# Kernel optimization log

Hardware: AMD Instinct MI355X
Metric: run time of the kernel (lower is better)

Reference implementation:

```python
import jax, jax.numpy as jnp
import numpy as np
import math

E = 16          # num_experts
K = 2           # top_k
CAP_FACTOR = 1.25
TEMP = 1.0      # router_temperature


def setup_inputs() -> dict:
    key = jax.random.key(0)
    ks = jax.random.split(key, 4)
    B, F, H, O = 16384, 1024, 4096, 1024
    features = jax.random.normal(ks[0], (B, F), dtype=jnp.float32)
    Wg = jax.random.normal(ks[1], (E, F), dtype=jnp.float32) / np.sqrt(F)
    bg = jnp.zeros((E,), jnp.float32)
    W1 = jax.random.normal(ks[2], (E, F, H), dtype=jnp.float32) / np.sqrt(F)
    b1 = jnp.zeros((E, H), jnp.float32)
    W2 = jax.random.normal(ks[3], (E, H, O), dtype=jnp.float32) / np.sqrt(H)
    b2 = jnp.zeros((E, O), jnp.float32)
    expert_bias = jnp.zeros((E,), jnp.float32)
    return {"features": features, "Wg": Wg, "bg": bg, "W1": W1, "b1": b1,
            "W2": W2, "b2": b2, "expert_bias": expert_bias}


def reference(features, Wg, bg, W1, b1, W2, b2, expert_bias):
    B, F = features.shape
    O = W2.shape[-1]
    cap = max(1, int(math.ceil(CAP_FACTOR * B * K / E)))  # per-expert capacity

    # --- router: scores = W_g * features + expert_bias (no noise) ---
    scores = features @ Wg.T + bg + expert_bias[None, :]            # [B,E]
    topk_scores, topk_idx = jax.lax.top_k(scores, K)                # [B,K]
    topk_w = jax.nn.softmax(topk_scores / TEMP, axis=1)             # [B,K]

    # per-(token,expert) assignment and mixing weight
    onehot = topk_idx[:, :, None] == jnp.arange(E)[None, None, :]   # [B,K,E]
    assign = jnp.any(onehot, axis=1)                                # [B,E]
    w = jnp.sum(topk_w[:, :, None] * onehot.astype(topk_w.dtype), axis=1)  # [B,E]

    # capacity: first `cap` tokens (ascending index, matching torch.nonzero order)
    pos = jnp.cumsum(assign.astype(jnp.int32), axis=0) - 1          # [B,E]
    keep = assign & (pos < cap)
    pos_safe = jnp.where(keep, pos, cap)                            # dropped -> overflow slot

    # inverse map: inv[e,c] = token index filling slot c of expert e (B if empty)
    e_grid = jnp.broadcast_to(jnp.arange(E)[None, :], (B, E))
    b_grid = jnp.broadcast_to(jnp.arange(B, dtype=jnp.int32)[:, None], (B, E))
    inv = jnp.full((E, cap + 1), B, dtype=jnp.int32)
    inv = inv.at[e_grid, pos_safe].set(b_grid)[:, :cap]             # [E,cap]

    # dispatch (gather) into per-expert buffers
    feats_pad = jnp.concatenate([features, jnp.zeros((1, F), features.dtype)], axis=0)
    buf = feats_pad[inv]                                            # [E,cap,F]

    # experts: Linear -> ReLU -> Linear, batched over experts
    h = jax.nn.relu(jnp.einsum('ecf,efh->ech', buf, W1) + b1[:, None, :])
    y = jnp.einsum('ech,eho->eco', h, W2) + b2[:, None, :]          # [E,cap,O]

    # weighted combine (scatter-add back to tokens; empty slots have weight 0)
    w_pad = jnp.concatenate([w, jnp.zeros((1, E), w.dtype)], axis=0)  # [B+1,E]
    w_slot = w_pad[inv, jnp.arange(E)[:, None]]                     # [E,cap]
    out = jnp.zeros((B + 1, O), features.dtype)
    out = out.at[inv.reshape(-1)].add((w_slot[..., None] * y).reshape(-1, O))
    return out[:B]
```

## Files before the change

### kernel.cpp

```cpp
#include <hip/hip_runtime.h>
#include <math.h>


typedef __attribute__((ext_vector_type(8))) short bf16x8;
typedef __attribute__((ext_vector_type(4))) float floatx4;

static __device__ __forceinline__ unsigned short f2bf(float f) {
  union { float f; unsigned u; } v; v.f = f;
  unsigned u = v.u;
  return (unsigned short)((u + 0x7fffu + ((u >> 16) & 1u)) >> 16);
}

static __device__ __forceinline__ void gload_lds16(const void* g, void* l) {
  __builtin_amdgcn_global_load_lds(
      (const __attribute__((address_space(1))) unsigned int*)g,
      (__attribute__((address_space(3))) unsigned int*)l, 16, 0, 0);
}

__global__ void k_cvt_bf16(const float* __restrict__ src,
                           unsigned short* __restrict__ dst, long n4) {
  long i = (long)blockIdx.x * blockDim.x + threadIdx.x;
  if (i >= n4) return;
  float4 f = ((const float4*)src)[i];
  ushort4 o;
  o.x = f2bf(f.x); o.y = f2bf(f.y); o.z = f2bf(f.z); o.w = f2bf(f.w);
  ((ushort4*)dst)[i] = o;
}

__global__ void k_txp_bf16(const float* __restrict__ src,
                           unsigned short* __restrict__ dst, int Kd, int Nd) {
  __shared__ float tile[32][33];
  int e = blockIdx.z;
  int n0 = blockIdx.x * 32;
  int k0 = blockIdx.y * 32;
  int tx = threadIdx.x;
  int ty = threadIdx.y;
  const float* s = src + (size_t)e * Kd * Nd;
#pragma unroll
  for (int j = 0; j < 4; ++j) {
    int k = ty + j * 8;
    tile[k][tx] = s[(size_t)(k0 + k) * Nd + n0 + tx];
  }
  __syncthreads();
  unsigned short* d = dst + (size_t)e * Kd * Nd;
#pragma unroll
  for (int j = 0; j < 4; ++j) {
    int n = ty + j * 8;
    d[(size_t)(n0 + n) * Kd + k0 + tx] = f2bf(tile[tx][n]);
  }
}

__global__ __launch_bounds__(256) void k_gating(
    const float* __restrict__ feat, const float* __restrict__ Wg,
    const float* __restrict__ bg, const float* __restrict__ ebias,
    int* __restrict__ topki, float* __restrict__ topkw,
    int* __restrict__ hist, int B, int F) {
  __shared__ float WgS[16 * 1024];
  for (int i = threadIdx.x; i < 16 * F; i += blockDim.x) WgS[i] = Wg[i];
  __syncthreads();
  int lane = threadIdx.x & 63;
  int wid = threadIdx.x >> 6;
  int gw = blockIdx.x * 4 + wid;
  int nw = gridDim.x * 4;
  int per = B / nw;
  for (int it = 0; it < per; ++it) {
    int t = gw * per + it;
    double acc[16];
#pragma unroll
    for (int e = 0; e < 16; ++e) acc[e] = 0.0;
    const float* fr = feat + (size_t)t * F;
    for (int c = 0; c < F / 64; ++c) {
      double fd = (double)fr[c * 64 + lane];
#pragma unroll
      for (int e = 0; e < 16; ++e)
        acc[e] += fd * (double)WgS[e * F + c * 64 + lane];
    }
#pragma unroll
    for (int e = 0; e < 16; ++e) {
#pragma unroll
      for (int off = 32; off >= 1; off >>= 1)
        acc[e] += __shfl_xor(acc[e], off);
    }
    double s[16];
#pragma unroll
    for (int e = 0; e < 16; ++e)
      s[e] = acc[e] + (double)bg[e] + (double)ebias[e];
    int e1 = 0; double s1 = s[0];
#pragma unroll
    for (int e = 1; e < 16; ++e) if (s[e] > s1) { s1 = s[e]; e1 = e; }
    int e2 = -1; double s2 = -1e300;
#pragma unroll
    for (int e = 0; e < 16; ++e)
      if (e != e1 && s[e] > s2) { s2 = s[e]; e2 = e; }
    double d = exp(s2 - s1);
    float w1 = (float)(1.0 / (1.0 + d));
    float w2 = (float)(d / (1.0 + d));
    if (lane == 0) {
      topki[t * 2 + 0] = e1; topki[t * 2 + 1] = e2;
      topkw[t * 2 + 0] = w1; topkw[t * 2 + 1] = w2;
      atomicAdd(&hist[(t >> 8) * 16 + e1], 1);
      atomicAdd(&hist[(t >> 8) * 16 + e2], 1);
    }
  }
}

__global__ void k_scan(const int* __restrict__ hist, int* __restrict__ choff,
                       int* __restrict__ cntcl, int nchunk, int cap) {
  int e = threadIdx.x;
  if (e < 16) {
    int off = 0;
    for (int c = 0; c < nchunk; ++c) {
      choff[c * 16 + e] = off;
      off += hist[c * 16 + e];
    }
    cntcl[e] = off < cap ? off : cap;
  }
}

__global__ __launch_bounds__(64) void k_build(
    const int* __restrict__ topki, const float* __restrict__ topkw,
    const int* __restrict__ choff, int* __restrict__ list,
    float* __restrict__ wlist, int cap, int capR) {
  int c = blockIdx.x;
  int lane = threadIdx.x;
  int run[16];
#pragma unroll
  for (int e = 0; e < 16; ++e) run[e] = choff[c * 16 + e];
  unsigned long long below = (lane == 63) ? 0x7fffffffffffffffull
                                          : ((1ull << lane) - 1ull);
  for (int r = 0; r < 4; ++r) {
    int t = c * 256 + r * 64 + lane;
    int e1 = topki[t * 2 + 0], e2 = topki[t * 2 + 1];
    float w1 = topkw[t * 2 + 0], w2 = topkw[t * 2 + 1];
    int p1 = -1, p2 = -1;
#pragma unroll
    for (int e = 0; e < 16; ++e) {
      unsigned long long m = __ballot(e1 == e) | __ballot(e2 == e);
      int rk = run[e] + __popcll(m & below);
      if (e1 == e) p1 = rk;
      if (e2 == e) p2 = rk;
      run[e] += __popcll(m);
    }
    if (p1 >= 0 && p1 < cap) { list[e1 * capR + p1] = t; wlist[e1 * capR + p1] = w1; }
    if (p2 >= 0 && p2 < cap) { list[e2 * capR + p2] = t; wlist[e2 * capR + p2] = w2; }
  }
}

__global__ void k_padfill(const int* __restrict__ cntcl, int* __restrict__ list,
                          float* __restrict__ wlist, int capR) {
  int e = blockIdx.x;
  int cnt = cntcl[e];
  for (int s = cnt + (int)threadIdx.x; s < capR; s += (int)blockDim.x) {
    list[e * capR + s] = 0;
    wlist[e * capR + s] = 0.0f;
  }
}

#define VM_WAIT4 asm volatile("s_waitcnt vmcnt(4)" ::: "memory")
#define VM_WAIT0 asm volatile("s_waitcnt vmcnt(0)" ::: "memory")

template <int MODE>
__global__ __launch_bounds__(512, 2) void k_gemm(
    const unsigned short* __restrict__ A, const unsigned short* __restrict__ Bt,
    const float* __restrict__ bias, const int* __restrict__ list,
    const float* __restrict__ wlist, const int* __restrict__ cntcl,
    unsigned short* __restrict__ Hout, float* __restrict__ out,
    int Kd, int Nd, int RT, int NT, int capR) {
  __shared__ __align__(16) char smem[131072];
  int bid = blockIdx.x;
  int e = bid / (RT * NT);
  int rt = (bid / NT) % RT;
  int nt = bid % NT;
  int cnt = cntcl[e];
  int r0 = rt * 256;
  if (r0 >= cnt) return;
  int n0 = nt * 256;

  int tid = threadIdx.x;
  int lane = tid & 63;
  int wid = tid >> 6;
  int wr = wid >> 2;
  int wc = wid & 3;
  int l16 = lane & 15, q = lane >> 4;

  const char* gA[2];
  const char* gB[2];
  int scg = lane & 3;
  int srl = lane >> 2;
#pragma unroll
  for (int p = 0; p < 2; ++p) {
    int r = (p * 8 + wid) * 16 + srl;
    int cgs = scg ^ ((r >> 1) & 3);
    const unsigned short* arow;
    if (MODE == 0) {
      int tok = list[e * capR + r0 + r];
      arow = A + (size_t)tok * Kd;
    } else {
      arow = A + (size_t)(e * capR + r0 + r) * Kd;
    }
    gA[p] = (const char*)arow + cgs * 16;
    const unsigned short* brow =
        Bt + (size_t)e * Nd * Kd + (size_t)(n0 + r) * Kd;
    gB[p] = (const char*)brow + cgs * 16;
  }
  int stofs[2];
#pragma unroll
  for (int p = 0; p < 2; ++p) stofs[p] = (p * 8 + wid) * 1024;

  floatx4 acc[8][4];
#pragma unroll
  for (int i = 0; i < 8; ++i)
#pragma unroll
    for (int j = 0; j < 4; ++j) acc[i][j] = 0.0f;

  int sw = ((q ^ ((lane >> 1) & 3)) << 4);
  int arl = wr * 128 + l16;
  int brl = wc * 64 + l16;

  int nk = Kd / 64;

#pragma unroll
  for (int p = 0; p < 2; ++p) gload_lds16(gA[p], smem + stofs[p]);
#pragma unroll
  for (int p = 0; p < 2; ++p) gload_lds16(gB[p], smem + 16384 + stofs[p]);
#pragma unroll
  for (int p = 0; p < 2; ++p) gload_lds16(gA[p] + 64, smem + 32768 + stofs[p]);
#pragma unroll
  for (int p = 0; p < 2; ++p) gload_lds16(gB[p] + 64, smem + 49152 + stofs[p]);
  VM_WAIT4;
  __builtin_amdgcn_s_barrier();

  bf16x8 af[8], bf[4];

  for (int t = 0; t < nk; ++t) {
    const char* Cb = smem + (t & 1) * 65536;
    char* Nb = smem + (((t & 1) ^ 1) * 65536);
    int gk = (t + 1) * 128;
    bool pre = (t + 1) < nk;

#pragma unroll
    for (int i = 0; i < 8; ++i)
      af[i] = *(const bf16x8*)(Cb + (arl + i * 16) * 64 + sw);
#pragma unroll
    for (int j = 0; j < 2; ++j)
      bf[j] = *(const bf16x8*)(Cb + 16384 + (brl + j * 16) * 64 + sw);
    if (pre) {
#pragma unroll
      for (int p = 0; p < 2; ++p) gload_lds16(gA[p] + gk, Nb + stofs[p]);
    }
    __builtin_amdgcn_s_barrier();
    __builtin_amdgcn_s_setprio(1);
#pragma unroll
    for (int j = 0; j < 2; ++j)
#pragma unroll
      for (int i = 0; i < 8; ++i)
        acc[i][j] = __builtin_amdgcn_mfma_f32_16x16x32_bf16(af[i], bf[j],
                                                            acc[i][j], 0, 0, 0);
    __builtin_amdgcn_s_setprio(0);
    __builtin_amdgcn_s_barrier();

#pragma unroll
    for (int j = 2; j < 4; ++j)
      bf[j] = *(const bf16x8*)(Cb + 16384 + (brl + j * 16) * 64 + sw);
    if (pre) {
#pragma unroll
      for (int p = 0; p < 2; ++p)
        gload_lds16(gB[p] + gk, Nb + 16384 + stofs[p]);
    }
    __builtin_amdgcn_s_barrier();
    __builtin_amdgcn_s_setprio(1);
#pragma unroll
    for (int j = 2; j < 4; ++j)
#pragma unroll
      for (int i = 0; i < 8; ++i)
        acc[i][j] = __builtin_amdgcn_mfma_f32_16x16x32_bf16(af[i], bf[j],
                                                            acc[i][j], 0, 0, 0);
    __builtin_amdgcn_s_setprio(0);
    if (pre) { VM_WAIT4; } else { VM_WAIT0; }
    __builtin_amdgcn_s_barrier();

#pragma unroll
    for (int i = 0; i < 8; ++i)
      af[i] = *(const bf16x8*)(Cb + 32768 + (arl + i * 16) * 64 + sw);
#pragma unroll
    for (int j = 0; j < 2; ++j)
      bf[j] = *(const bf16x8*)(Cb + 49152 + (brl + j * 16) * 64 + sw);
    if (pre) {
#pragma unroll
      for (int p = 0; p < 2; ++p)
        gload_lds16(gA[p] + gk + 64, Nb + 32768 + stofs[p]);
    }
    __builtin_amdgcn_s_barrier();
    __builtin_amdgcn_s_setprio(1);
#pragma unroll
    for (int j = 0; j < 2; ++j)
#pragma unroll
      for (int i = 0; i < 8; ++i)
        acc[i][j] = __builtin_amdgcn_mfma_f32_16x16x32_bf16(af[i], bf[j],
                                                            acc[i][j], 0, 0, 0);
    __builtin_amdgcn_s_setprio(0);
    __builtin_amdgcn_s_barrier();

#pragma unroll
    for (int j = 2; j < 4; ++j)
      bf[j] = *(const bf16x8*)(Cb + 49152 + (brl + j * 16) * 64 + sw);
    if (pre) {
#pragma unroll
      for (int p = 0; p < 2; ++p)
        gload_lds16(gB[p] + gk + 64, Nb + 49152 + stofs[p]);
    }
    __builtin_amdgcn_s_barrier();
    __builtin_amdgcn_s_setprio(1);
#pragma unroll
    for (int j = 2; j < 4; ++j)
#pragma unroll
      for (int i = 0; i < 8; ++i)
        acc[i][j] = __builtin_amdgcn_mfma_f32_16x16x32_bf16(af[i], bf[j],
                                                            acc[i][j], 0, 0, 0);
    __builtin_amdgcn_s_setprio(0);
    if (pre) { VM_WAIT4; }
    __builtin_amdgcn_s_barrier();
  }

  float bv[4];
#pragma unroll
  for (int j = 0; j < 4; ++j)
    bv[j] = bias[(size_t)e * Nd + n0 + wc * 64 + j * 16 + l16];

  if (MODE == 0) {
#pragma unroll
    for (int i = 0; i < 8; ++i) {
      int rowb = r0 + wr * 128 + i * 16 + q * 4;
#pragma unroll
      for (int j = 0; j < 4; ++j) {
        int col = n0 + wc * 64 + j * 16 + l16;
#pragma unroll
        for (int r = 0; r < 4; ++r) {
          float v = acc[i][j][r] + bv[j];
          v = v > 0.0f ? v : 0.0f;
          Hout[(size_t)(e * capR + rowb + r) * Nd + col] = f2bf(v);
        }
      }
    }
  } else {
#pragma unroll
    for (int i = 0; i < 8; ++i) {
      int rowb = r0 + wr * 128 + i * 16 + q * 4;
      int tok[4]; float wv[4];
#pragma unroll
      for (int r = 0; r < 4; ++r) {
        tok[r] = list[e * capR + rowb + r];
        wv[r] = wlist[e * capR + rowb + r];
      }
#pragma unroll
      for (int j = 0; j < 4; ++j) {
        int col = n0 + wc * 64 + j * 16 + l16;
#pragma unroll
        for (int r = 0; r < 4; ++r) {
          float v = (acc[i][j][r] + bv[j]) * wv[r];
          atomicAdd(&out[(size_t)tok[r] * Nd + col], v);
        }
      }
    }
  }
}

extern "C" void kernel_launch(void* const* d_in, const int* in_sizes, int n_in,
                              void* d_out, int out_size, void* d_ws,
                              size_t ws_size, hipStream_t stream) {
  const float* feat  = (const float*)d_in[0];
  const float* Wg    = (const float*)d_in[1];
  const float* bg    = (const float*)d_in[2];
  const float* W1    = (const float*)d_in[3];
  const float* b1    = (const float*)d_in[4];
  const float* W2    = (const float*)d_in[5];
  const float* b2    = (const float*)d_in[6];
  const float* ebias = (const float*)d_in[7];

  const int E = 16;
  const int B = 16384, F = 1024, Hd = 4096, O = 1024;
  const int cap = 2560;
  const int capR = 2560;
  const int nchunk = B / 256;
  const int RT = capR / 256;

  char* p = (char*)d_ws;
  auto carve = [&](size_t bytes) {
    char* r = p;
    p += (bytes + 255) & ~(size_t)255;
    return r;
  };
  unsigned short* featbf = (unsigned short*)carve((size_t)B * F * 2);
  unsigned short* W1T = (unsigned short*)carve((size_t)E * Hd * F * 2);
  unsigned short* W2T = (unsigned short*)carve((size_t)E * O * Hd * 2);
  unsigned short* Hbuf = (unsigned short*)carve((size_t)E * capR * Hd * 2);
  int* topki = (int*)carve((size_t)B * 2 * 4);
  float* topkw = (float*)carve((size_t)B * 2 * 4);
  int* hist = (int*)carve((size_t)nchunk * 16 * 4);
  int* choff = (int*)carve((size_t)nchunk * 16 * 4);
  int* cntcl = (int*)carve(16 * 4);
  int* list = (int*)carve((size_t)E * capR * 4);
  float* wlist = (float*)carve((size_t)E * capR * 4);

  hipMemsetAsync(d_out, 0, (size_t)B * O * sizeof(float), stream);
  hipMemsetAsync(hist, 0, (size_t)nchunk * 16 * 4, stream);

  k_cvt_bf16<<<(B * F / 4 + 255) / 256, 256, 0, stream>>>(feat, featbf,
                                                          (long)B * F / 4);
  dim3 tb(32, 8);
  k_txp_bf16<<<dim3(Hd / 32, F / 32, E), tb, 0, stream>>>(W1, W1T, F, Hd);
  k_txp_bf16<<<dim3(O / 32, Hd / 32, E), tb, 0, stream>>>(W2, W2T, Hd, O);
  k_gating<<<256, 256, 0, stream>>>(feat, Wg, bg, ebias, topki, topkw, hist, B, F);
  k_scan<<<1, 64, 0, stream>>>(hist, choff, cntcl, nchunk, cap);
  k_build<<<nchunk, 64, 0, stream>>>(topki, topkw, choff, list, wlist, cap, capR);
  k_padfill<<<E, 256, 0, stream>>>(cntcl, list, wlist, capR);

  k_gemm<0><<<E * RT * (Hd / 256), 512, 0, stream>>>(
      featbf, W1T, b1, list, wlist, cntcl, Hbuf, nullptr, F, Hd, RT, Hd / 256,
      capR);
  k_gemm<1><<<E * RT * (O / 256), 512, 0, stream>>>(
      Hbuf, W2T, b2, list, wlist, cntcl, nullptr, (float*)d_out, Hd, O, RT,
      O / 256, capR);
}
```

Before: 1.710 ms.

## Switch GEMM to 3-stage K32 LDS pipeline and XCD-aware block remap

Rewrites the expert GEMM main loop from a double-buffered 64-wide-K step (two 32-K halves) to a triple-buffered ring of 32-K stages. Loads run two stages ahead with fewer barriers per stage, and LDS drops from 128KB to 96KB. It also remaps block IDs so that consecutive logical tiles land on the same XCD, which should improve L2 reuse of expert weights. The risks are more loop iterations with per-stage barrier overhead, and the wait counts must match the shallower loads per stage.

```diff
diff --git a/kernel.cpp b/kernel.cpp
--- a/kernel.cpp
+++ b/kernel.cpp
@@ -166,8 +166,13 @@
     const float* __restrict__ wlist, const int* __restrict__ cntcl,
     unsigned short* __restrict__ Hout, float* __restrict__ out,
     int Kd, int Nd, int RT, int NT, int capR) {
-  __shared__ __align__(16) char smem[131072];
-  int bid = blockIdx.x;
+  __shared__ __align__(16) char smem[98304];
+
+  int nwg = gridDim.x;
+  int qq = nwg >> 3, rr = nwg & 7;
+  int xcd = blockIdx.x & 7, idx = blockIdx.x >> 3;
+  int bid = (xcd < rr ? xcd * (qq + 1) : rr * (qq + 1) + (xcd - rr) * qq) + idx;
+
   int e = bid / (RT * NT);
   int rt = (bid / NT) % RT;
   int nt = bid % NT;
@@ -183,14 +188,13 @@
   int wc = wid & 3;
   int l16 = lane & 15, q = lane >> 4;
 
-  const char* gA[2];
-  const char* gB[2];
-  int scg = lane & 3;
-  int srl = lane >> 2;
-#pragma unroll
-  for (int p = 0; p < 2; ++p) {
-    int r = (p * 8 + wid) * 16 + srl;
-    int cgs = scg ^ ((r >> 1) & 3);
+  int srow = wid * 16 + (lane >> 2);
+  int cg = (lane & 3) ^ ((lane >> 3) & 3);
+  const char* pA[2];
+  const char* pB[2];
+#pragma unroll
+  for (int rnd = 0; rnd < 2; ++rnd) {
+    int r = rnd * 128 + srow;
     const unsigned short* arow;
     if (MODE == 0) {
       int tok = list[e * capR + r0 + r];
@@ -198,14 +202,21 @@
     } else {
       arow = A + (size_t)(e * capR + r0 + r) * Kd;
     }
-    gA[p] = (const char*)arow + cgs * 16;
-    const unsigned short* brow =
-        Bt + (size_t)e * Nd * Kd + (size_t)(n0 + r) * Kd;
-    gB[p] = (const char*)brow + cgs * 16;
-  }
-  int stofs[2];
-#pragma unroll
-  for (int p = 0; p < 2; ++p) stofs[p] = (p * 8 + wid) * 1024;
+    pA[rnd] = (const char*)arow + cg * 16;
+    pB[rnd] = (const char*)(Bt + (size_t)e * Nd * Kd + (size_t)(n0 + r) * Kd) +
+              cg * 16;
+  }
+  unsigned stbase = wid * 1024;
+
+#define STAGE(tt, bufi)                                   \
+  do {                                                    \
+    char* dst_ = smem + (bufi) * 32768 + stbase;          \
+    int off_ = (tt) * 64;                                 \
+    gload_lds16(pA[0] + off_, dst_);                      \
+    gload_lds16(pA[1] + off_, dst_ + 8192);               \
+    gload_lds16(pB[0] + off_, dst_ + 16384);              \
+    gload_lds16(pB[1] + off_, dst_ + 16384 + 8192);       \
+  } while (0)
 
   floatx4 acc[8][4];
 #pragma unroll
@@ -217,110 +228,57 @@
   int arl = wr * 128 + l16;
   int brl = wc * 64 + l16;
 
-  int nk = Kd / 64;
-
-#pragma unroll
-  for (int p = 0; p < 2; ++p) gload_lds16(gA[p], smem + stofs[p]);
-#pragma unroll
-  for (int p = 0; p < 2; ++p) gload_lds16(gB[p], smem + 16384 + stofs[p]);
-#pragma unroll
-  for (int p = 0; p < 2; ++p) gload_lds16(gA[p] + 64, smem + 32768 + stofs[p]);
-#pragma unroll
-  for (int p = 0; p < 2; ++p) gload_lds16(gB[p] + 64, smem + 49152 + stofs[p]);
+  int nk = Kd / 32;
+
+  STAGE(0, 0);
+  STAGE(1, 1);
   VM_WAIT4;
   __builtin_amdgcn_s_barrier();
 
-  bf16x8 af[8], bf[4];
-
+  int cur = 0;
   for (int t = 0; t < nk; ++t) {
-    const char* Cb = smem + (t & 1) * 65536;
-    char* Nb = smem + (((t & 1) ^ 1) * 65536);
-    int gk = (t + 1) * 128;
-    bool pre = (t + 1) < nk;
-
-#pragma unroll
-    for (int i = 0; i < 8; ++i)
-      af[i] = *(const bf16x8*)(Cb + (arl + i * 16) * 64 + sw);
-#pragma unroll
-    for (int j = 0; j < 2; ++j)
-      bf[j] = *(const bf16x8*)(Cb + 16384 + (brl + j * 16) * 64 + sw);
-    if (pre) {
-#pragma unroll
-      for (int p = 0; p < 2; ++p) gload_lds16(gA[p] + gk, Nb + stofs[p]);
-    }
+    const char* Ab = smem + cur * 32768;
+    const char* Bb = Ab + 16384;
+    bool pre = (t + 2) < nk;
+    int nx2 = cur + 2; if (nx2 >= 3) nx2 -= 3;
+
+    bf16x8 af[4], bfr[4];
+#pragma unroll
+    for (int i = 0; i < 4; ++i)
+      af[i] = *(const bf16x8*)(Ab + (arl + i * 16) * 64 + sw);
+#pragma unroll
+    for (int j = 0; j < 4; ++j)
+      bfr[j] = *(const bf16x8*)(Bb + (brl + j * 16) * 64 + sw);
+    if (pre) STAGE(t + 2, nx2);
     __builtin_amdgcn_s_barrier();
     __builtin_amdgcn_s_setprio(1);
 #pragma unroll
-    for (int j = 0; j < 2; ++j)
-#pragma unroll
-      for (int i = 0; i < 8; ++i)
-        acc[i][j] = __builtin_amdgcn_mfma_f32_16x16x32_bf16(af[i], bf[j],
+    for (int i = 0; i < 4; ++i)
+#pragma unroll
+      for (int j = 0; j < 4; ++j)
+        acc[i][j] = __builtin_amdgcn_mfma_f32_16x16x32_bf16(af[i], bfr[j],
                                                             acc[i][j], 0, 0, 0);
     __builtin_amdgcn_s_setprio(0);
     __builtin_amdgcn_s_barrier();
 
-#pragma unroll
-    for (int j = 2; j < 4; ++j)
-      bf[j] = *(const bf16x8*)(Cb + 16384 + (brl + j * 16) * 64 + sw);
-    if (pre) {
-#pragma unroll
-      for (int p = 0; p < 2; ++p)
-        gload_lds16(gB[p] + gk, Nb + 16384 + stofs[p]);
-    }
+    bf16x8 ag[4];
+#pragma unroll
+    for (int i = 0; i < 4; ++i)
+      ag[i] = *(const bf16x8*)(Ab + (arl + 64 + i * 16) * 64 + sw);
     __builtin_amdgcn_s_barrier();
     __builtin_amdgcn_s_setprio(1);
 #pragma unroll
-    for (int j = 2; j < 4; ++j)
-#pragma unroll
-      for (int i = 0; i < 8; ++i)
-        acc[i][j] = __builtin_amdgcn_mfma_f32_16x16x32_bf16(af[i], bf[j],
-                                                            acc[i][j], 0, 0, 0);
+    for (int i = 0; i < 4; ++i)
+#pragma unroll
+      for (int j = 0; j < 4; ++j)
+        acc[4 + i][j] = __builtin_amdgcn_mfma_f32_16x16x32_bf16(
+            ag[i], bfr[j], acc[4 + i][j], 0, 0, 0);
     __builtin_amdgcn_s_setprio(0);
     if (pre) { VM_WAIT4; } else { VM_WAIT0; }
     __builtin_amdgcn_s_barrier();
-
-#pragma unroll
-    for (int i = 0; i < 8; ++i)
-      af[i] = *(const bf16x8*)(Cb + 32768 + (arl + i * 16) * 64 + sw);
-#pragma unroll
-    for (int j = 0; j < 2; ++j)
-      bf[j] = *(const bf16x8*)(Cb + 49152 + (brl + j * 16) * 64 + sw);
-    if (pre) {
-#pragma unroll
-      for (int p = 0; p < 2; ++p)
-        gload_lds16(gA[p] + gk + 64, Nb + 32768 + stofs[p]);
-    }
-    __builtin_amdgcn_s_barrier();
-    __builtin_amdgcn_s_setprio(1);
-#pragma unroll
-    for (int j = 0; j < 2; ++j)
-#pragma unroll
-      for (int i = 0; i < 8; ++i)
-        acc[i][j] = __builtin_amdgcn_mfma_f32_16x16x32_bf16(af[i], bf[j],
-                                                            acc[i][j], 0, 0, 0);
-    __builtin_amdgcn_s_setprio(0);
-    __builtin_amdgcn_s_barrier();
-
-#pragma unroll
-    for (int j = 2; j < 4; ++j)
-      bf[j] = *(const bf16x8*)(Cb + 49152 + (brl + j * 16) * 64 + sw);
-    if (pre) {
-#pragma unroll
-      for (int p = 0; p < 2; ++p)
-        gload_lds16(gB[p] + gk + 64, Nb + 49152 + stofs[p]);
-    }
-    __builtin_amdgcn_s_barrier();
-    __builtin_amdgcn_s_setprio(1);
-#pragma unroll
-    for (int j = 2; j < 4; ++j)
-#pragma unroll
-      for (int i = 0; i < 8; ++i)
-        acc[i][j] = __builtin_amdgcn_mfma_f32_16x16x32_bf16(af[i], bf[j],
-                                                            acc[i][j], 0, 0, 0);
-    __builtin_amdgcn_s_setprio(0);
-    if (pre) { VM_WAIT4; }
-    __builtin_amdgcn_s_barrier();
-  }
+    cur = (cur + 1 == 3) ? 0 : cur + 1;
+  }
+#undef STAGE
 
   float bv[4];
 #pragma unroll
```

New measurement: 1.760 ms. 1.03x slower.
